# Kernel optimization log

Measured on AMD Instinct MI355X. Metric: run time of the kernel, lower is better.

Reference implementation:

```python
import jax, jax.numpy as jnp
import numpy as np

B, S, H1, H2, D4, LAT, DD1, DD2, K = 8192, 4096, 196, 10, 1024, 32, 1024, 2048, 21

def _knn_mask(rng, rows, cols, k):
    # disjoint-group style mask: each column has exactly k ones (as produced by knnLayer's non-overlap grouping)
    m = np.zeros((rows, cols), dtype=np.float32)
    order = np.argsort(rng.random((rows, cols)), axis=0)[:k]  # [k, cols]
    m[order, np.arange(cols)[None, :]] = 1.0
    return m

def _glorot(rng, shape):
    lim = np.sqrt(6.0 / (shape[0] + shape[1]))
    return (rng.uniform(-lim, lim, size=shape)).astype(np.float32)

def setup_inputs() -> dict:
    rng = np.random.default_rng(0)
    key = jax.random.key(0)
    x = jax.random.uniform(key, (B, S), dtype=jnp.float32)
    inp = {
        'x': x,
        'C1': jnp.asarray(_knn_mask(rng, S, H1, K)),
        'W1': jnp.asarray(_glorot(rng, (S, H1))),
        'b1': jnp.zeros((H1,), jnp.float32),
        'C2': jnp.asarray(_knn_mask(rng, H1, H2, K)),
        'W2': jnp.asarray(_glorot(rng, (H1, H2))),
        'b2': jnp.zeros((H2,), jnp.float32),
        'W3': jnp.asarray(_glorot(rng, (H2, D4))),
        'b3': jnp.zeros((D4,), jnp.float32),
        'W4': jnp.asarray(_glorot(rng, (D4, LAT))),
        'b4': jnp.zeros((LAT,), jnp.float32),
        'Wd1': jnp.asarray(_glorot(rng, (LAT, DD1))),
        'bd1': jnp.zeros((DD1,), jnp.float32),
        'Wd2': jnp.asarray(_glorot(rng, (DD1, DD2))),
        'bd2': jnp.zeros((DD2,), jnp.float32),
        'Wd3': jnp.asarray(_glorot(rng, (DD2, S))),
        'bd3': jnp.zeros((S,), jnp.float32),
    }
    return inp

def reference(x, C1, W1, b1, C2, W2, b2, W3, b3, W4, b4, Wd1, bd1, Wd2, bd2, Wd3, bd3):
    # encoder: two masked (CustomConnected) layers + two dense layers
    h = jax.nn.relu(x @ (W1 * C1) + b1)            # [B, H1]
    h = jax.nn.relu(h @ (W2 * C2) + b2)            # [B, H2]
    h = jax.nn.relu(h @ W3 + b3)                    # [B, S/4]
    z = jax.nn.relu(h @ W4 + b4)                    # [B, latent]
    # decoder: relu, relu, sigmoid
    d = jax.nn.relu(z @ Wd1 + bd1)                  # [B, S/4]
    d = jax.nn.relu(d @ Wd2 + bd2)                  # [B, S/2]
    out = jax.nn.sigmoid(d @ Wd3 + bd3)             # [B, S]
    return out
```

## Files before the change

### kernel.cpp

```cpp
#include <hip/hip_runtime.h>
#include <hip/hip_fp8.h>
#include <cstdint>
#include <cstddef>

typedef __attribute__((ext_vector_type(4))) float f32x4;
typedef __attribute__((ext_vector_type(8))) int i32x8;

#define DEVINL __device__ __forceinline__

DEVINL unsigned short f2bf(float f){
  union { float f; unsigned u; } v; v.f = f;
  unsigned r = v.u + 0x7fffu + ((v.u >> 16) & 1u);
  return (unsigned short)(r >> 16);
}
DEVINL float bf2f(unsigned short h){
  union { unsigned u; float f; } v; v.u = ((unsigned)h) << 16;
  return v.f;
}
DEVINL unsigned char f2fp8(float f){
  __hip_fp8_e4m3 t(f);
  return (unsigned char)t.__x;
}
DEVINL void gload_lds16(const void* g, void* l){
  __builtin_amdgcn_global_load_lds((const __attribute__((address_space(1))) void*)g,
                                   (__attribute__((address_space(3))) void*)l, 16, 0, 0);
}

#define ACT_SCALE 64.0f
#define W_SCALE   16.0f
#define E8M0_ACT  121
#define E8M0_W    123

__global__ __launch_bounds__(256) void transpose_fp8(
    const float* __restrict__ W, unsigned char* __restrict__ Wt, int K, int N)
{
  __shared__ unsigned char tile[32][33];
  int k0 = blockIdx.x * 32, n0 = blockIdx.y * 32;
  int tx = threadIdx.x & 31, ty = threadIdx.x >> 5;
  #pragma unroll
  for (int i = 0; i < 4; ++i) {
    int k = k0 + ty + 8*i, n = n0 + tx;
    tile[ty + 8*i][tx] = f2fp8(W[(size_t)k*N + n] * W_SCALE);
  }
  __syncthreads();
  #pragma unroll
  for (int i = 0; i < 4; ++i) {
    int n = n0 + ty + 8*i, k = k0 + tx;
    Wt[(size_t)n*K + k] = tile[tx][ty + 8*i];
  }
}

__global__ __launch_bounds__(256) void build_sparse(
    const float* __restrict__ C1, const float* __restrict__ W1,
    unsigned* __restrict__ packed)
{
  const int j = blockIdx.x;
  const int w = threadIdx.x >> 6, l = threadIdx.x & 63;
  __shared__ int wcnt[4], wbase[4];
  int cnt = 0;
  #pragma unroll 4
  for (int it = 0; it < 16; ++it) {
    int k = w*1024 + it*64 + l;
    float c = C1[(size_t)k*196 + j];
    unsigned long long m = __ballot(c != 0.f);
    cnt += (int)__popcll(m);
  }
  if (l == 0) wcnt[w] = cnt;
  __syncthreads();
  if (threadIdx.x < 21) packed[j*21 + threadIdx.x] = 0;
  if (threadIdx.x == 0) {
    int b = 0;
    #pragma unroll
    for (int i = 0; i < 4; ++i) { wbase[i] = b; b += wcnt[i]; }
  }
  __syncthreads();
  int base = wbase[w];
  #pragma unroll 4
  for (int it = 0; it < 16; ++it) {
    int k = w*1024 + it*64 + l;
    float c = C1[(size_t)k*196 + j];
    unsigned long long m = __ballot(c != 0.f);
    if (c != 0.f) {
      int pos = base + (int)__popcll(m & ((1ull << l) - 1ull));
      if (pos < 21)
        packed[j*21 + pos] = ((unsigned)k << 16)
                           | (unsigned)f2bf(W1[(size_t)k*196 + j] * c);
    }
    base += (int)__popcll(m);
  }
}

__global__ __launch_bounds__(256) void layer1_sparse(
    const float* __restrict__ x, const unsigned* __restrict__ packed,
    const float* __restrict__ b1, unsigned short* __restrict__ h1)
{
  __shared__ __align__(16) float xs[2*4096];
  const int t = threadIdx.x;
  const long m0 = (long)blockIdx.x * 2;
  const char* src = (const char*)(x + m0*4096);
  #pragma unroll
  for (int i = 0; i < 8; ++i) {
    int seg = t + i*256;
    gload_lds16(src + (size_t)seg*16, (char*)xs + (size_t)seg*16);
  }
  __syncthreads();
  for (int e = t; e < 2*196; e += 256) {
    int row = (e >= 196) ? 1 : 0;
    int col = e - row*196;
    const float* xr = xs + row*4096;
    float acc = b1[col];
    #pragma unroll
    for (int i = 0; i < 21; ++i) {
      unsigned p = packed[col*21 + i];
      acc += xr[p >> 16] * bf2f((unsigned short)(p & 0xffffu));
    }
    h1[(m0 + row)*256 + col] = f2bf(fmaxf(acc, 0.f));
  }
}

template<int ACT>
__global__ __launch_bounds__(256) void gemm_fp8(
    const unsigned char* __restrict__ A, const unsigned char* __restrict__ Bt,
    const float* __restrict__ bias, void* __restrict__ Cptr, int K, int ldC)
{
  constexpr int BM = 128, BN = 128, BK = 128;
  constexpr int HM = 64, HN = 64, FM = 4, FN = 4;
  __shared__ __align__(16) unsigned char smem[32768];
  unsigned char* As = smem;
  unsigned char* Bs = smem + 16384;
  const int tid  = threadIdx.x;
  const int lane = tid & 63;
  const int w    = tid >> 6;
  const int wm = w & 1, wn = w >> 1;
  const int q = lane >> 4, l16 = lane & 15;
  const long m0 = (long)blockIdx.x * BM;
  const long n0 = (long)blockIdx.y * BN;

  f32x4 acc[FM][FN] = {};

  for (int k0 = 0; k0 < K; k0 += BK) {
    #pragma unroll
    for (int it = 0; it < 4; ++it) {
      int seg = tid + it*256;
      int row = seg >> 3;
      int g   = (5*(seg & 7) + 3*row) & 7;
      gload_lds16(A + (m0 + row)*(long)K + k0 + g*16, As + seg*16);
    }
    #pragma unroll
    for (int it = 0; it < 4; ++it) {
      int seg = tid + it*256;
      int row = seg >> 3;
      int g   = (5*(seg & 7) + 3*row) & 7;
      gload_lds16(Bt + (n0 + row)*(long)K + k0 + g*16, Bs + seg*16);
    }
    __syncthreads();

    i32x8 a[FM], b[FN];
    #pragma unroll
    for (int i = 0; i < FM; ++i) {
      int r = wm*HM + i*16 + l16;
      const uint4* p = (const uint4*)(As + r*BK);
      int c0 = (2*q + r) & 7;
      union { uint4 v[2]; i32x8 f; } u;
      u.v[0] = p[c0];
      u.v[1] = p[(c0 + 5) & 7];
      a[i] = u.f;
    }
    #pragma unroll
    for (int j = 0; j < FN; ++j) {
      int r = wn*HN + j*16 + l16;
      const uint4* p = (const uint4*)(Bs + r*BK);
      int c0 = (2*q + r) & 7;
      union { uint4 v[2]; i32x8 f; } u;
      u.v[0] = p[c0];
      u.v[1] = p[(c0 + 5) & 7];
      b[j] = u.f;
    }
    #pragma unroll
    for (int i = 0; i < FM; ++i)
      #pragma unroll
      for (int j = 0; j < FN; ++j)
        acc[i][j] = __builtin_amdgcn_mfma_scale_f32_16x16x128_f8f6f4(
            a[i], b[j], acc[i][j], 0, 0, 0, E8M0_ACT, 0, E8M0_W);
    __syncthreads();
  }

  if constexpr (ACT == 0) {
    #pragma unroll
    for (int j = 0; j < FN; ++j) {
      int cl = wn*HN + j*16 + l16;
      float bv = bias[n0 + cl];
      #pragma unroll
      for (int i = 0; i < FM; ++i) {
        #pragma unroll
        for (int r = 0; r < 4; ++r) {
          int rl = wm*HM + i*16 + q*4 + r;
          smem[rl*144 + cl] = f2fp8(fmaxf(acc[i][j][r] + bv, 0.f) * ACT_SCALE);
        }
      }
    }
    __syncthreads();
    unsigned char* C = (unsigned char*)Cptr;
    #pragma unroll
    for (int it = 0; it < 4; ++it) {
      int seg = tid + it*256;
      int row = seg >> 3;
      *(uint4*)(C + (m0 + row)*(long)ldC + n0 + (seg & 7)*16) =
          *(const uint4*)(smem + row*144 + (seg & 7)*16);
    }
  } else {
    float* C = (float*)Cptr;
    #pragma unroll
    for (int j = 0; j < FN; ++j) {
      long col = n0 + wn*HN + j*16 + l16;
      float bv = bias[col];
      #pragma unroll
      for (int i = 0; i < FM; ++i) {
        #pragma unroll
        for (int r = 0; r < 4; ++r) {
          long row = m0 + wm*HM + i*16 + q*4 + r;
          float v = acc[i][j][r] + bv;
          C[row*(long)ldC + col] = 1.f / (1.f + __expf(-v));
        }
      }
    }
  }
}

__global__ __launch_bounds__(256) void layer2345(
    const unsigned short* __restrict__ h1,
    const float* __restrict__ W2, const float* __restrict__ C2, const float* __restrict__ b2,
    const float* __restrict__ W3, const float* __restrict__ b3,
    const float* __restrict__ W4, const float* __restrict__ b4,
    const float* __restrict__ Wd1, const float* __restrict__ bd1,
    unsigned char* __restrict__ d1)
{
  __shared__ float h1s[4][200];
  __shared__ float h2s[4][10];
  __shared__ float h3s[4][1024];
  __shared__ float part[8][128];
  __shared__ float zs[4][32];
  const int t = threadIdx.x;
  const int w = t >> 6, l = t & 63;
  const long m0 = (long)blockIdx.x * 4;

  for (int e = t; e < 4*196; e += 256) {
    int row = e / 196, col = e - row*196;
    h1s[row][col] = bf2f(h1[(m0 + row)*256 + col]);
  }
  __syncthreads();

  {
    float acc[10];
    #pragma unroll
    for (int n = 0; n < 10; ++n) acc[n] = 0.f;
    #pragma unroll
    for (int it = 0; it < 4; ++it) {
      int k = l + it*64;
      if (k < 196) {
        float a = h1s[w][k];
        #pragma unroll
        for (int n = 0; n < 10; ++n) acc[n] += a * W2[k*10 + n] * C2[k*10 + n];
      }
    }
    #pragma unroll
    for (int off = 32; off > 0; off >>= 1) {
      #pragma unroll
      for (int n = 0; n < 10; ++n) acc[n] += __shfl_down(acc[n], off, 64);
    }
    if (l < 10) h2s[w][l] = fmaxf(acc[l] + b2[l], 0.f);
  }
  __syncthreads();

  #pragma unroll
  for (int jj = 0; jj < 4; ++jj) {
    int n = w*256 + jj*64 + l;
    float a0 = b3[n], a1 = a0, a2 = a0, a3 = a0;
    #pragma unroll
    for (int k = 0; k < 10; ++k) {
      float wv = W3[k*1024 + n];
      a0 += h2s[0][k]*wv; a1 += h2s[1][k]*wv;
      a2 += h2s[2][k]*wv; a3 += h2s[3][k]*wv;
    }
    h3s[0][n] = fmaxf(a0, 0.f); h3s[1][n] = fmaxf(a1, 0.f);
    h3s[2][n] = fmaxf(a2, 0.f); h3s[3][n] = fmaxf(a3, 0.f);
  }
  __syncthreads();

  {
    int n = t & 31, kg = t >> 5;
    float a0 = 0.f, a1 = 0.f, a2 = 0.f, a3 = 0.f;
    for (int k = kg*128; k < kg*128 + 128; ++k) {
      float wv = W4[k*32 + n];
      a0 += h3s[0][k]*wv; a1 += h3s[1][k]*wv;
      a2 += h3s[2][k]*wv; a3 += h3s[3][k]*wv;
    }
    part[kg][0*32 + n] = a0; part[kg][1*32 + n] = a1;
    part[kg][2*32 + n] = a2; part[kg][3*32 + n] = a3;
  }
  __syncthreads();
  if (t < 128) {
    float s = 0.f;
    #pragma unroll
    for (int kg = 0; kg < 8; ++kg) s += part[kg][t];
    zs[t >> 5][t & 31] = fmaxf(s + b4[t & 31], 0.f);
  }
  __syncthreads();

  #pragma unroll
  for (int jj = 0; jj < 4; ++jj) {
    int n = w*256 + jj*64 + l;
    float a0 = bd1[n], a1 = a0, a2 = a0, a3 = a0;
    #pragma unroll
    for (int k = 0; k < 32; ++k) {
      float wv = Wd1[k*1024 + n];
      a0 += zs[0][k]*wv; a1 += zs[1][k]*wv;
      a2 += zs[2][k]*wv; a3 += zs[3][k]*wv;
    }
    d1[(m0 + 0)*1024 + n] = f2fp8(fmaxf(a0, 0.f) * ACT_SCALE);
    d1[(m0 + 1)*1024 + n] = f2fp8(fmaxf(a1, 0.f) * ACT_SCALE);
    d1[(m0 + 2)*1024 + n] = f2fp8(fmaxf(a2, 0.f) * ACT_SCALE);
    d1[(m0 + 3)*1024 + n] = f2fp8(fmaxf(a3, 0.f) * ACT_SCALE);
  }
}

extern "C" void kernel_launch(void* const* d_in, const int* in_sizes, int n_in,
                              void* d_out, int out_size, void* d_ws, size_t ws_size,
                              hipStream_t stream)
{
  (void)in_sizes; (void)n_in; (void)out_size; (void)ws_size;
  const float* x   = (const float*)d_in[0];
  const float* C1  = (const float*)d_in[1];
  const float* W1  = (const float*)d_in[2];
  const float* b1  = (const float*)d_in[3];
  const float* C2  = (const float*)d_in[4];
  const float* W2  = (const float*)d_in[5];
  const float* b2  = (const float*)d_in[6];
  const float* W3  = (const float*)d_in[7];
  const float* b3  = (const float*)d_in[8];
  const float* W4  = (const float*)d_in[9];
  const float* b4  = (const float*)d_in[10];
  const float* Wd1 = (const float*)d_in[11];
  const float* bd1 = (const float*)d_in[12];
  const float* Wd2 = (const float*)d_in[13];
  const float* bd2 = (const float*)d_in[14];
  const float* Wd3 = (const float*)d_in[15];
  const float* bd3 = (const float*)d_in[16];
  float* out = (float*)d_out;

  char* ws = (char*)d_ws;
  size_t off = 0;
  auto alloc = [&](size_t bytes) -> void* {
    void* p = ws + off; off += (bytes + 255) & ~(size_t)255; return p;
  };
  unsigned char* Wt2 = (unsigned char*)alloc((size_t)2048*1024);
  unsigned char* Wt3 = (unsigned char*)alloc((size_t)4096*2048);
  unsigned*      pk  = (unsigned*)     alloc((size_t)196*21*4);
  unsigned short* h1 = (unsigned short*)alloc((size_t)8192*256*2);
  unsigned char*  d1 = (unsigned char*) alloc((size_t)8192*1024);
  unsigned char*  d2 = (unsigned char*) alloc((size_t)8192*2048);

  build_sparse<<<dim3(196), 256, 0, stream>>>(C1, W1, pk);
  transpose_fp8<<<dim3(1024/32, 2048/32), 256, 0, stream>>>(Wd2, Wt2, 1024, 2048);
  transpose_fp8<<<dim3(2048/32, 4096/32), 256, 0, stream>>>(Wd3, Wt3, 2048, 4096);

  layer1_sparse<<<dim3(8192/2), 256, 0, stream>>>(x, pk, b1, h1);
  layer2345<<<dim3(8192/4), 256, 0, stream>>>(h1, W2, C2, b2, W3, b3, W4, b4,
                                              Wd1, bd1, d1);
  gemm_fp8<0><<<dim3(8192/128, 2048/128), 256, 0, stream>>>(
      d1, Wt2, bd2, d2, 1024, 2048);
  gemm_fp8<1><<<dim3(8192/128, 4096/128), 256, 0, stream>>>(
      d2, Wt3, bd3, out, 2048, 4096);
}
```

Before: 462.9 us.

## Widen FP8 GEMM tile to 128x256 with per-wave 128x64 subtiles

```diff
diff --git a/kernel.cpp b/kernel.cpp
--- a/kernel.cpp
+++ b/kernel.cpp
@@ -119,19 +119,18 @@
 }
 
 template<int ACT>
-__global__ __launch_bounds__(256) void gemm_fp8(
+__global__ __launch_bounds__(256, 2) void gemm_fp8(
     const unsigned char* __restrict__ A, const unsigned char* __restrict__ Bt,
     const float* __restrict__ bias, void* __restrict__ Cptr, int K, int ldC)
 {
-  constexpr int BM = 128, BN = 128, BK = 128;
-  constexpr int HM = 64, HN = 64, FM = 4, FN = 4;
-  __shared__ __align__(16) unsigned char smem[32768];
+  constexpr int BM = 128, BN = 256, BK = 128;
+  constexpr int FM = 8, FN = 4;
+  __shared__ __align__(16) unsigned char smem[49152];
   unsigned char* As = smem;
   unsigned char* Bs = smem + 16384;
   const int tid  = threadIdx.x;
   const int lane = tid & 63;
   const int w    = tid >> 6;
-  const int wm = w & 1, wn = w >> 1;
   const int q = lane >> 4, l16 = lane & 15;
   const long m0 = (long)blockIdx.x * BM;
   const long n0 = (long)blockIdx.y * BN;
@@ -147,7 +146,7 @@
       gload_lds16(A + (m0 + row)*(long)K + k0 + g*16, As + seg*16);
     }
     #pragma unroll
-    for (int it = 0; it < 4; ++it) {
+    for (int it = 0; it < 8; ++it) {
       int seg = tid + it*256;
       int row = seg >> 3;
       int g   = (5*(seg & 7) + 3*row) & 7;
@@ -155,20 +154,10 @@
     }
     __syncthreads();
 
-    i32x8 a[FM], b[FN];
-    #pragma unroll
-    for (int i = 0; i < FM; ++i) {
-      int r = wm*HM + i*16 + l16;
-      const uint4* p = (const uint4*)(As + r*BK);
-      int c0 = (2*q + r) & 7;
-      union { uint4 v[2]; i32x8 f; } u;
-      u.v[0] = p[c0];
-      u.v[1] = p[(c0 + 5) & 7];
-      a[i] = u.f;
-    }
+    i32x8 b[FN];
     #pragma unroll
     for (int j = 0; j < FN; ++j) {
-      int r = wn*HN + j*16 + l16;
+      int r = w*64 + j*16 + l16;
       const uint4* p = (const uint4*)(Bs + r*BK);
       int c0 = (2*q + r) & 7;
       union { uint4 v[2]; i32x8 f; } u;
@@ -177,48 +166,56 @@
       b[j] = u.f;
     }
     #pragma unroll
-    for (int i = 0; i < FM; ++i)
+    for (int i = 0; i < FM; ++i) {
+      int r = i*16 + l16;
+      const uint4* p = (const uint4*)(As + r*BK);
+      int c0 = (2*q + r) & 7;
+      union { uint4 v[2]; i32x8 f; } u;
+      u.v[0] = p[c0];
+      u.v[1] = p[(c0 + 5) & 7];
+      i32x8 a = u.f;
       #pragma unroll
       for (int j = 0; j < FN; ++j)
         acc[i][j] = __builtin_amdgcn_mfma_scale_f32_16x16x128_f8f6f4(
-            a[i], b[j], acc[i][j], 0, 0, 0, E8M0_ACT, 0, E8M0_W);
+            a, b[j], acc[i][j], 0, 0, 0, E8M0_ACT, 0, E8M0_W);
+    }
     __syncthreads();
   }
 
   if constexpr (ACT == 0) {
     #pragma unroll
     for (int j = 0; j < FN; ++j) {
-      int cl = wn*HN + j*16 + l16;
+      int cl = w*64 + j*16 + l16;
       float bv = bias[n0 + cl];
       #pragma unroll
       for (int i = 0; i < FM; ++i) {
         #pragma unroll
         for (int r = 0; r < 4; ++r) {
-          int rl = wm*HM + i*16 + q*4 + r;
-          smem[rl*144 + cl] = f2fp8(fmaxf(acc[i][j][r] + bv, 0.f) * ACT_SCALE);
+          int rl = i*16 + q*4 + r;
+          smem[rl*272 + cl] = f2fp8(fmaxf(acc[i][j][r] + bv, 0.f) * ACT_SCALE);
         }
       }
     }
     __syncthreads();
     unsigned char* C = (unsigned char*)Cptr;
     #pragma unroll
-    for (int it = 0; it < 4; ++it) {
+    for (int it = 0; it < 8; ++it) {
       int seg = tid + it*256;
-      int row = seg >> 3;
-      *(uint4*)(C + (m0 + row)*(long)ldC + n0 + (seg & 7)*16) =
-          *(const uint4*)(smem + row*144 + (seg & 7)*16);
+      int row = seg >> 4, ch = seg & 15;
+      *(uint4*)(C + (m0 + row)*(long)ldC + n0 + ch*16) =
+          *(const uint4*)(smem + row*272 + ch*16);
     }
   } else {
     float* C = (float*)Cptr;
     #pragma unroll
     for (int j = 0; j < FN; ++j) {
-      long col = n0 + wn*HN + j*16 + l16;
+      long col = n0 + w*64 + j*16 + l16;
       float bv = bias[col];
       #pragma unroll
       for (int i = 0; i < FM; ++i) {
         #pragma unroll
         for (int r = 0; r < 4; ++r) {
-          long row = m0 + wm*HM + i*16 + q*4 + r;
+          long row = m0 + i*16 + q*4 + r;
           float v = acc[i][j][r] + bv;
           C[row*(long)ldC + col] = 1.f / (1.f + __expf(-v));
         }
@@ -367,8 +364,8 @@
   layer1_sparse<<<dim3(8192/2), 256, 0, stream>>>(x, pk, b1, h1);
   layer2345<<<dim3(8192/4), 256, 0, stream>>>(h1, W2, C2, b2, W3, b3, W4, b4,
                                               Wd1, bd1, d1);
-  gemm_fp8<0><<<dim3(8192/128, 2048/128), 256, 0, stream>>>(
+  gemm_fp8<0><<<dim3(8192/128, 2048/256), 256, 0, stream>>>(
       d1, Wt2, bd2, d2, 1024, 2048);
-  gemm_fp8<1><<<dim3(8192/128, 4096/128), 256, 0, stream>>>(
+  gemm_fp8<1><<<dim3(8192/128, 4096/256), 256, 0, stream>>>(
       d2, Wt3, bd3, out, 2048, 4096);
 }
```

New measurement: 458.7 us. Within noise of the previous version (-0.9%).
